# Kernel optimization log

Measured on AMD Instinct MI355X. Metric: run time of the kernel, lower is better.

## Reference

```python
import jax, jax.numpy as jnp
import numpy as np

N, D, H, E = 50000, 128, 64, 800000


def _linear_params(key, fan_in, fan_out):
    k1, k2 = jax.random.split(key)
    bound = 1.0 / np.sqrt(fan_in)
    w = jax.random.uniform(k1, (fan_in, fan_out), jnp.float32, -bound, bound)
    b = jax.random.uniform(k2, (fan_out,), jnp.float32, -bound, bound)
    return w, b


def setup_inputs() -> dict:
    key = jax.random.key(0)
    ks = jax.random.split(key, 10)
    node_states = jax.random.normal(ks[0], (N, D), jnp.float32)
    capacities = jax.random.uniform(ks[1], (N,), jnp.float32)
    edge_index = jax.random.randint(ks[2], (2, E), 0, N, jnp.int64)
    # redistribution_net: Linear(2D->H), SiLU, Linear(H->H), SiLU, Linear(H->1)
    rw1, rb1 = _linear_params(ks[3], 2 * D, H)
    rw2, rb2 = _linear_params(ks[4], H, H)
    rw3, rb3 = _linear_params(ks[5], H, 1)
    # protection_net: Linear(D+1->H), SiLU, Linear(H->1)
    pw1, pb1 = _linear_params(ks[6], D + 1, H)
    pw2, pb2 = _linear_params(ks[7], H, 1)
    # post_jump_transform: Linear(D->D), Tanh
    tw, tb = _linear_params(ks[8], D, D)
    return dict(node_states=node_states, capacities=capacities, edge_index=edge_index,
                rw1=rw1, rb1=rb1, rw2=rw2, rb2=rb2, rw3=rw3, rb3=rb3,
                pw1=pw1, pb1=pb1, pw2=pw2, pb2=pb2, tw=tw, tb=tb)


def reference(node_states, capacities, edge_index,
              rw1, rb1, rw2, rb2, rw3, rb3,
              pw1, pb1, pw2, pb2, tw, tb):
    n = node_states.shape[0]
    # --- detect_jumps: protection_net(cat(states, capacities)) > 0 ---
    x = jnp.concatenate([node_states, capacities[:, None]], axis=-1)  # (N, D+1)
    act = (jax.nn.silu(x @ pw1 + pb1) @ pw2 + pb2)[:, 0]              # (N,)
    jump_mask = act > 0.0

    # --- redistribute_load ---
    src, tgt = edge_index[0], edge_index[1]
    src_failed = jump_mask[src]
    tgt_alive = ~jump_mask[tgt]
    emask = src_failed & tgt_alive                                    # (E,)

    wi = jnp.concatenate([node_states[src], node_states[tgt]], axis=-1)  # (E, 2D)
    h = jax.nn.silu(wi @ rw1 + rb1)
    h = jax.nn.silu(h @ rw2 + rb2)
    raw = (h @ rw3 + rb3)[:, 0]                                       # (E,)

    # per-source segment softmax over edges with emask
    raw_m = jnp.where(emask, raw, -jnp.inf)
    seg_max = jax.ops.segment_max(raw_m, src, num_segments=n)
    seg_max = jnp.where(jnp.isfinite(seg_max), seg_max, 0.0)
    e = jnp.where(emask, jnp.exp(raw - seg_max[src]), 0.0)
    denom = jax.ops.segment_sum(e, src, num_segments=n)
    dsrc = denom[src]
    w = e / jnp.where(dsrc > 0, dsrc, 1.0)                            # (E,)

    failed_load = jnp.where(jump_mask[:, None], node_states, 0.0)     # (N, D)
    messages = w[:, None] * failed_load[src]                          # (E, D)
    added = jax.ops.segment_sum(messages, tgt, num_segments=n)        # (N, D)
    redistributed = node_states + added

    # --- apply_jumps: failed nodes -> tanh(Linear(x)) * 0.05 ---
    protected = jnp.tanh(redistributed @ tw + tb) * 0.05
    new_states = jnp.where(jump_mask[:, None], protected, redistributed)
    return new_states, jump_mask
```

## Files before the change

kernel.cpp:

```cpp
#include <hip/hip_runtime.h>
#include <cmath>

#define D 128
#define HID 64

__device__ __forceinline__ float silu_f(float x) { return x / (1.0f + expf(-x)); }

__device__ __forceinline__ float4 fma4(float a, float4 w, float4 c) {
    c.x = fmaf(a, w.x, c.x); c.y = fmaf(a, w.y, c.y);
    c.z = fmaf(a, w.z, c.z); c.w = fmaf(a, w.w, c.w);
    return c;
}
__device__ __forceinline__ float4 silu4(float4 v) {
    v.x = silu_f(v.x); v.y = silu_f(v.y); v.z = silu_f(v.z); v.w = silu_f(v.w);
    return v;
}

__device__ __forceinline__ unsigned fenc(float f) {
    unsigned u = __float_as_uint(f);
    return (u & 0x80000000u) ? ~u : (u | 0x80000000u);
}
__device__ __forceinline__ float fdec(unsigned e) {
    unsigned u = (e & 0x80000000u) ? (e & 0x7FFFFFFFu) : ~e;
    return __uint_as_float(u);
}

#define INIT16(bp) { const float4* _b4 = reinterpret_cast<const float4*>(bp); \
    h0 = _b4[0]; h1 = _b4[1]; h2 = _b4[2]; h3 = _b4[3]; \
    h4 = _b4[4]; h5 = _b4[5]; h6 = _b4[6]; h7 = _b4[7]; \
    h8 = _b4[8]; h9 = _b4[9]; h10 = _b4[10]; h11 = _b4[11]; \
    h12 = _b4[12]; h13 = _b4[13]; h14 = _b4[14]; h15 = _b4[15]; }

#define SILU16() { h0 = silu4(h0); h1 = silu4(h1); h2 = silu4(h2); h3 = silu4(h3); \
    h4 = silu4(h4); h5 = silu4(h5); h6 = silu4(h6); h7 = silu4(h7); \
    h8 = silu4(h8); h9 = silu4(h9); h10 = silu4(h10); h11 = silu4(h11); \
    h12 = silu4(h12); h13 = silu4(h13); h14 = silu4(h14); h15 = silu4(h15); }

__device__ __forceinline__ void fd4(float4 h, float4 w, float& s0, float& s1, float& s2, float& s3) {
    s0 = fmaf(h.x, w.x, s0); s1 = fmaf(h.y, w.y, s1);
    s2 = fmaf(h.z, w.z, s2); s3 = fmaf(h.w, w.w, s3);
}
#define FD16(w4) { fd4(h0, w4[0], s0, s1, s2, s3);  fd4(h1, w4[1], s0, s1, s2, s3);  \
    fd4(h2, w4[2], s0, s1, s2, s3);  fd4(h3, w4[3], s0, s1, s2, s3);  \
    fd4(h4, w4[4], s0, s1, s2, s3);  fd4(h5, w4[5], s0, s1, s2, s3);  \
    fd4(h6, w4[6], s0, s1, s2, s3);  fd4(h7, w4[7], s0, s1, s2, s3);  \
    fd4(h8, w4[8], s0, s1, s2, s3);  fd4(h9, w4[9], s0, s1, s2, s3);  \
    fd4(h10, w4[10], s0, s1, s2, s3); fd4(h11, w4[11], s0, s1, s2, s3); \
    fd4(h12, w4[12], s0, s1, s2, s3); fd4(h13, w4[13], s0, s1, s2, s3); \
    fd4(h14, w4[14], s0, s1, s2, s3); fd4(h15, w4[15], s0, s1, s2, s3); }

__device__ __forceinline__ float accdot(float4 h, float4 w, float act) {
    act = fmaf(silu_f(h.x), w.x, act);
    act = fmaf(silu_f(h.y), w.y, act);
    act = fmaf(silu_f(h.z), w.z, act);
    act = fmaf(silu_f(h.w), w.w, act);
    return act;
}

__global__ void k_prep(const float* __restrict__ rw2, float* __restrict__ rw2T) {
    int i = blockIdx.x * blockDim.x + threadIdx.x;
    if (i < HID * HID) rw2T[i] = rw2[(i & (HID - 1)) * HID + (i >> 6)];
}

__global__ __launch_bounds__(256) void k_protect(
    const float* __restrict__ states, const float* __restrict__ caps,
    const float* __restrict__ pw1, const float* __restrict__ pb1,
    const float* __restrict__ pw2, const float* __restrict__ pb2,
    unsigned* __restrict__ mask, unsigned* __restrict__ mlist,
    unsigned* __restrict__ counters, float* __restrict__ outmask, int N) {
    __shared__ float wl[129 * 64];
    unsigned tid = threadIdx.x;
    {
        const float4* s4 = reinterpret_cast<const float4*>(pw1);
        float4* d4 = reinterpret_cast<float4*>(wl);
#pragma unroll
        for (int q = 0; q < 9; ++q) {
            unsigned idx = tid + q * 256u;
            if (idx < 2064u) d4[idx] = s4[idx];
        }
    }
    __syncthreads();
    unsigned nl = tid >> 2, g = tid & 3u;
    unsigned n = blockIdx.x * 64u + nl;
    bool active = n < (unsigned)N;
    unsigned nq = active ? n : (unsigned)(N - 1);
    const float4* row = reinterpret_cast<const float4*>(states + (size_t)nq * D);
    float4 a0, a1, a2, a3;
    { const float4* b4 = reinterpret_cast<const float4*>(pb1 + g * 16);
      a0 = b4[0]; a1 = b4[1]; a2 = b4[2]; a3 = b4[3]; }
    const float* wg = wl + g * 16;
#pragma unroll 4
    for (int kb = 0; kb < 32; ++kb) {
        float4 x = row[kb];
        const float* w = wg + (size_t)kb * 4 * HID;
        const float4* w0 = reinterpret_cast<const float4*>(w);
        const float4* w1 = reinterpret_cast<const float4*>(w + HID);
        const float4* w2q = reinterpret_cast<const float4*>(w + 2 * HID);
        const float4* w3q = reinterpret_cast<const float4*>(w + 3 * HID);
        a0 = fma4(x.x, w0[0], a0); a1 = fma4(x.x, w0[1], a1); a2 = fma4(x.x, w0[2], a2); a3 = fma4(x.x, w0[3], a3);
        a0 = fma4(x.y, w1[0], a0); a1 = fma4(x.y, w1[1], a1); a2 = fma4(x.y, w1[2], a2); a3 = fma4(x.y, w1[3], a3);
        a0 = fma4(x.z, w2q[0], a0); a1 = fma4(x.z, w2q[1], a1); a2 = fma4(x.z, w2q[2], a2); a3 = fma4(x.z, w2q[3], a3);
        a0 = fma4(x.w, w3q[0], a0); a1 = fma4(x.w, w3q[1], a1); a2 = fma4(x.w, w3q[2], a2); a3 = fma4(x.w, w3q[3], a3);
    }
    {
        float xv = caps[nq];
        const float4* wc = reinterpret_cast<const float4*>(wg + (size_t)128 * HID);
        a0 = fma4(xv, wc[0], a0); a1 = fma4(xv, wc[1], a1);
        a2 = fma4(xv, wc[2], a2); a3 = fma4(xv, wc[3], a3);
    }
    const float4* w2 = reinterpret_cast<const float4*>(pw2 + g * 16);
    float p = 0.0f;
    p = accdot(a0, w2[0], p); p = accdot(a1, w2[1], p);
    p = accdot(a2, w2[2], p); p = accdot(a3, w2[3], p);
    p += __shfl_xor(p, 1);
    p += __shfl_xor(p, 2);
    bool pred = false;
    if (active && g == 0) {
        float act = p + pb2[0];
        unsigned m = (act > 0.0f) ? 1u : 0u;
        mask[n] = m;
        outmask[n] = m ? 1.0f : 0.0f;
        pred = (m != 0u);
    }
    unsigned lane = tid & 63u;
    unsigned long long bal = __ballot(pred);
    unsigned wcnt = (unsigned)__popcll(bal);
    unsigned pre  = (unsigned)__popcll(bal & ((1ull << lane) - 1ull));
    unsigned base = 0;
    if (lane == 0 && wcnt) base = atomicAdd(&counters[1], wcnt);
    base = __shfl(base, 0);
    if (pred) mlist[base + pre] = n;
}

__global__ __launch_bounds__(256) void k_nodemlp(
    const float* __restrict__ states, const unsigned* __restrict__ mask,
    const float* __restrict__ rw1, float* __restrict__ uv, int N) {
    __shared__ float wl[16384];
    unsigned tid = threadIdx.x;
    {
        const float4* s4 = reinterpret_cast<const float4*>(rw1);
        float4* d4 = reinterpret_cast<float4*>(wl);
#pragma unroll
        for (int q = 0; q < 16; ++q) d4[tid + q * 256u] = s4[tid + q * 256u];
    }
    __syncthreads();
    unsigned nl = tid >> 2, g = tid & 3u;
    unsigned n = blockIdx.x * 64u + nl;
    if (n >= (unsigned)N) return;
    const float4* row = reinterpret_cast<const float4*>(states + (size_t)n * D);
    unsigned m = mask[n];
    const float* wg = wl + (m ? 0u : 8192u) + g * 16;
    float4 a0, a1, a2, a3;
    a0.x=a0.y=a0.z=a0.w=0.f; a1=a0; a2=a0; a3=a0;
#pragma unroll 4
    for (int kb = 0; kb < 32; ++kb) {
        float4 x = row[kb];
        const float* w = wg + (size_t)kb * 4 * HID;
        const float4* w0 = reinterpret_cast<const float4*>(w);
        const float4* w1 = reinterpret_cast<const float4*>(w + HID);
        const float4* w2q = reinterpret_cast<const float4*>(w + 2 * HID);
        const float4* w3q = reinterpret_cast<const float4*>(w + 3 * HID);
        a0 = fma4(x.x, w0[0], a0); a1 = fma4(x.x, w0[1], a1); a2 = fma4(x.x, w0[2], a2); a3 = fma4(x.x, w0[3], a3);
        a0 = fma4(x.y, w1[0], a0); a1 = fma4(x.y, w1[1], a1); a2 = fma4(x.y, w1[2], a2); a3 = fma4(x.y, w1[3], a3);
        a0 = fma4(x.z, w2q[0], a0); a1 = fma4(x.z, w2q[1], a1); a2 = fma4(x.z, w2q[2], a2); a3 = fma4(x.z, w2q[3], a3);
        a0 = fma4(x.w, w3q[0], a0); a1 = fma4(x.w, w3q[1], a1); a2 = fma4(x.w, w3q[2], a2); a3 = fma4(x.w, w3q[3], a3);
    }
    float4* o = reinterpret_cast<float4*>(uv + (size_t)n * HID + g * 16);
    o[0] = a0; o[1] = a1; o[2] = a2; o[3] = a3;
}

__global__ __launch_bounds__(256) void k_compact(
    const int* __restrict__ ei, const unsigned* __restrict__ mask,
    unsigned* __restrict__ act_eid, unsigned* __restrict__ counters,
    unsigned* __restrict__ hist, int E) {
    __shared__ unsigned wbase[4];
    int e = blockIdx.x * 256 + threadIdx.x;
    unsigned wid = threadIdx.x >> 6, lane = threadIdx.x & 63u;
    bool pred = false; int t = 0;
    if (e < E) {
        int s = ei[e]; t = ei[E + e];
        pred = mask[s] && !mask[t];
    }
    unsigned long long bal = __ballot(pred);
    unsigned wcnt = (unsigned)__popcll(bal);
    unsigned pre  = (unsigned)__popcll(bal & ((1ull << lane) - 1ull));
    if (lane == 0) wbase[wid] = wcnt;
    __syncthreads();
    if (threadIdx.x == 0) {
        unsigned c0 = wbase[0], c1 = wbase[1], c2 = wbase[2], c3 = wbase[3];
        unsigned tot = c0 + c1 + c2 + c3;
        unsigned b = tot ? atomicAdd(&counters[0], tot) : 0u;
        wbase[0] = b; wbase[1] = b + c0; wbase[2] = b + c0 + c1; wbase[3] = b + c0 + c1 + c2;
    }
    __syncthreads();
    if (pred) {
        act_eid[wbase[wid] + pre] = (unsigned)e;
        atomicAdd(&hist[t], 1u);
    }
}

__global__ __launch_bounds__(256) void k_scanA(const unsigned* __restrict__ hist,
                                               unsigned* __restrict__ bsum, int N) {
    __shared__ unsigned sm[256];
    unsigned t = threadIdx.x;
    unsigned i = blockIdx.x * 256u + t;
    sm[t] = (i < (unsigned)N) ? hist[i] : 0u;
    __syncthreads();
#pragma unroll
    for (unsigned d = 128; d > 0; d >>= 1) {
        if (t < d) sm[t] += sm[t + d];
        __syncthreads();
    }
    if (t == 0) bsum[blockIdx.x] = sm[0];
}
__global__ __launch_bounds__(256) void k_scanB(const unsigned* __restrict__ bsum,
                                               unsigned* __restrict__ bpre, int nb) {
    __shared__ unsigned sm[256];
    unsigned t = threadIdx.x;
    unsigned v = (t < (unsigned)nb) ? bsum[t] : 0u;
    sm[t] = v;
    __syncthreads();
    for (unsigned d = 1; d < 256; d <<= 1) {
        unsigned x = (t >= d) ? sm[t - d] : 0u;
        __syncthreads();
        sm[t] += x;
        __syncthreads();
    }
    if (t < (unsigned)nb) bpre[t] = sm[t] - v;
}
__global__ __launch_bounds__(256) void k_scanC(const unsigned* __restrict__ hist,
                                               const unsigned* __restrict__ bpre,
                                               unsigned* __restrict__ offs,
                                               unsigned* __restrict__ cursor, int N) {
    __shared__ unsigned sm[256];
    unsigned t = threadIdx.x;
    unsigned i = blockIdx.x * 256u + t;
    unsigned v = (i < (unsigned)N) ? hist[i] : 0u;
    sm[t] = v;
    __syncthreads();
    for (unsigned d = 1; d < 256; d <<= 1) {
        unsigned x = (t >= d) ? sm[t - d] : 0u;
        __syncthreads();
        sm[t] += x;
        __syncthreads();
    }
    unsigned exc = sm[t] - v + bpre[blockIdx.x];
    if (i < (unsigned)N) { offs[i] = exc; cursor[i] = exc; }
    if (i == (unsigned)N - 1) offs[N] = exc + v;
}

__global__ __launch_bounds__(256) void k_edge_mlp(
    const float* __restrict__ uv, const int* __restrict__ ei,
    const float* __restrict__ rb1, const float* __restrict__ rw2T,
    const float* __restrict__ rb2, const float* __restrict__ rw3,
    const float* __restrict__ rb3,
    const unsigned* __restrict__ act_eid, const unsigned* __restrict__ counters,
    float* __restrict__ rawbuf, unsigned* __restrict__ segmax, int E) {
    unsigned cnt = counters[0];
    if (blockIdx.x * 256u >= cnt) return;
    unsigned tid = threadIdx.x;
    unsigned grp = blockIdx.x * 256u + tid;
    bool active = grp < cnt;
    unsigned gq = active ? grp : (cnt - 1);
    int e = (int)act_eid[gq];
    int s = ei[e], tg = ei[E + e];
    const float4* ur = reinterpret_cast<const float4*>(uv + (size_t)s * HID);
    const float4* vr = reinterpret_cast<const float4*>(uv + (size_t)tg * HID);
    float4 h0, h1, h2, h3, h4, h5, h6, h7, h8, h9, h10, h11, h12, h13, h14, h15;
    INIT16(rb1);
#define ADDUV(hh, i) { float4 _u = ur[i]; float4 _v = vr[i]; \
    hh.x = hh.x + _u.x + _v.x; hh.y = hh.y + _u.y + _v.y; \
    hh.z = hh.z + _u.z + _v.z; hh.w = hh.w + _u.w + _v.w; }
    ADDUV(h0, 0)  ADDUV(h1, 1)  ADDUV(h2, 2)  ADDUV(h3, 3)
    ADDUV(h4, 4)  ADDUV(h5, 5)  ADDUV(h6, 6)  ADDUV(h7, 7)
    ADDUV(h8, 8)  ADDUV(h9, 9)  ADDUV(h10, 10) ADDUV(h11, 11)
    ADDUV(h12, 12) ADDUV(h13, 13) ADDUV(h14, 14) ADDUV(h15, 15)
#undef ADDUV
    SILU16();
    float raw = rb3[0];
#pragma unroll 1
    for (int j = 0; j < HID; ++j) {
        const float4* w4 = reinterpret_cast<const float4*>(rw2T + (size_t)j * HID);
        float s0 = rb2[j], s1 = 0.f, s2 = 0.f, s3 = 0.f;
        FD16(w4);
        float h2v = silu_f((s0 + s1) + (s2 + s3));
        raw = fmaf(h2v, rw3[j], raw);
    }
    if (active) {
        rawbuf[grp] = raw;
        atomicMax(&segmax[s], fenc(raw));
    }
}

__global__ void k_expfill(const int* __restrict__ ei, const unsigned* __restrict__ act_eid,
                          const unsigned* __restrict__ counters, const unsigned* __restrict__ segmax,
                          const float* __restrict__ rawbuf, float* __restrict__ denom,
                          unsigned* __restrict__ cursor,
                          float* __restrict__ wbuf, unsigned* __restrict__ sbuf, int E) {
    unsigned t = blockIdx.x * blockDim.x + threadIdx.x;
    if (blockIdx.x * blockDim.x >= counters[0]) return;
    if (t >= counters[0]) return;
    int e = (int)act_eid[t];
    int s = ei[e], tg = ei[E + e];
    float ev = expf(rawbuf[t] - fdec(segmax[s]));
    atomicAdd(&denom[s], ev);
    unsigned pos = atomicAdd(&cursor[tg], 1u);
    wbuf[pos] = ev;
    sbuf[pos] = (unsigned)s;
}

__global__ __launch_bounds__(256) void k_gather(
    const float* __restrict__ states, const float* __restrict__ wbuf,
    const unsigned* __restrict__ sbuf, const unsigned* __restrict__ offs,
    const float* __restrict__ denom, const unsigned* __restrict__ mask,
    float* __restrict__ out, int N) {
    unsigned n = blockIdx.x * 4u + (threadIdx.x >> 6);
    unsigned lane = threadIdx.x & 63u;
    if (n >= (unsigned)N) return;
    if (mask[n]) return;
    unsigned start = offs[n], end = offs[n + 1];
    float2 acc = reinterpret_cast<const float2*>(states + (size_t)n * D)[lane];
    for (unsigned i = start; i < end; ++i) {
        unsigned s = sbuf[i];
        float w = wbuf[i] / denom[s];
        float2 sv = reinterpret_cast<const float2*>(states + (size_t)s * D)[lane];
        acc.x = fmaf(w, sv.x, acc.x);
        acc.y = fmaf(w, sv.y, acc.y);
    }
    reinterpret_cast<float2*>(out + (size_t)n * D)[lane] = acc;
}

__global__ __launch_bounds__(256) void k_jump(
    const float* __restrict__ states,
    const float* __restrict__ tw, const float* __restrict__ tb,
    const unsigned* __restrict__ mlist, const unsigned* __restrict__ counters,
    float* __restrict__ out) {
    __shared__ float xs[8][D];
    unsigned cnt = counters[1];
    unsigned base = blockIdx.x * 8u;
    if (base >= cnt || cnt == 0) return;
    unsigned tid = threadIdx.x;
    unsigned d = tid & 127u, r = tid >> 7;
    {
        unsigned j = tid >> 5;
        unsigned c = (tid & 31u) * 4u;
        unsigned slot = base + j; if (slot >= cnt) slot = cnt - 1;
        int nn = (int)mlist[slot];
        *reinterpret_cast<float4*>(&xs[j][c]) =
            *reinterpret_cast<const float4*>(&states[(size_t)nn * D + c]);
    }
    __syncthreads();
    float tbd = tb[d];
    float a0 = tbd, a1 = tbd, a2 = tbd, a3 = tbd;
    const float* x0 = &xs[r * 4 + 0][0];
    const float* x1 = &xs[r * 4 + 1][0];
    const float* x2 = &xs[r * 4 + 2][0];
    const float* x3 = &xs[r * 4 + 3][0];
#pragma unroll 1
    for (int k = 0; k < D; ++k) {
        float w = tw[(size_t)k * D + d];
        a0 = fmaf(x0[k], w, a0);
        a1 = fmaf(x1[k], w, a1);
        a2 = fmaf(x2[k], w, a2);
        a3 = fmaf(x3[k], w, a3);
    }
    float res[4] = {a0, a1, a2, a3};
#pragma unroll
    for (int j2 = 0; j2 < 4; ++j2) {
        unsigned slot = base + r * 4 + j2;
        if (slot < cnt) {
            int nn = (int)mlist[slot];
            out[(size_t)nn * D + d] = tanhf(res[j2]) * 0.05f;
        }
    }
}

extern "C" void kernel_launch(void* const* d_in, const int* in_sizes, int n_in,
                              void* d_out, int out_size, void* d_ws, size_t ws_size,
                              hipStream_t stream) {
    const float* states = (const float*)d_in[0];
    const float* caps   = (const float*)d_in[1];
    const int*   ei     = (const int*)d_in[2];
    const float* rw1 = (const float*)d_in[3];  const float* rb1 = (const float*)d_in[4];
    const float* rw2 = (const float*)d_in[5];  const float* rb2 = (const float*)d_in[6];
    const float* rw3 = (const float*)d_in[7];  const float* rb3 = (const float*)d_in[8];
    const float* pw1 = (const float*)d_in[9];  const float* pb1 = (const float*)d_in[10];
    const float* pw2 = (const float*)d_in[11]; const float* pb2 = (const float*)d_in[12];
    const float* tw  = (const float*)d_in[13]; const float* tb  = (const float*)d_in[14];
    const int N = in_sizes[1];
    const int E = in_sizes[2] / 2;
    float* out = (float*)d_out;
    const int nb = (N + 255) / 256;

    float* uv = out;

    unsigned* ws       = (unsigned*)d_ws;
    unsigned* counters = ws;
    unsigned* segmax   = ws + 4;
    float*    denom    = (float*)(ws + 4 + 1 * (size_t)N);
    unsigned* hist     = ws + 4 + 2 * (size_t)N;
    unsigned* mask     = ws + 4 + 3 * (size_t)N;
    unsigned* mlist    = ws + 4 + 4 * (size_t)N;
    unsigned* offs     = ws + 4 + 5 * (size_t)N;
    unsigned* cursor   = ws + 4 + 6 * (size_t)N + 1;
    unsigned* bsum     = ws + 4 + 7 * (size_t)N + 1;
    unsigned* bpre     = bsum + 256;
    unsigned* act_eid  = bpre + 256;
    float*    rawbuf   = (float*)(act_eid + (size_t)E);
    float*    wbuf     = (float*)(act_eid + 2 * (size_t)E);
    unsigned* sbuf     = act_eid + 3 * (size_t)E;
    float*    rw2T     = (float*)(act_eid + 4 * (size_t)E);

    (void)hipMemsetAsync(d_ws, 0, (size_t)(4 + 3 * (size_t)N) * 4, stream);

    k_prep<<<(HID * HID + 255) / 256, 256, 0, stream>>>(rw2, rw2T);
    k_protect<<<(N + 63) / 64, 256, 0, stream>>>(states, caps, pw1, pb1, pw2, pb2,
                                                 mask, mlist, counters, out + (size_t)N * D, N);
    k_nodemlp<<<(N + 63) / 64, 256, 0, stream>>>(states, mask, rw1, uv, N);
    k_compact<<<(E + 255) / 256, 256, 0, stream>>>(ei, mask, act_eid, counters, hist, E);
    k_scanA<<<nb, 256, 0, stream>>>(hist, bsum, N);
    k_scanB<<<1, 256, 0, stream>>>(bsum, bpre, nb);
    k_scanC<<<nb, 256, 0, stream>>>(hist, bpre, offs, cursor, N);
    k_edge_mlp<<<(E + 255) / 256, 256, 0, stream>>>(uv, ei, rb1, rw2T, rb2, rw3, rb3,
                                                    act_eid, counters, rawbuf, segmax, E);
    k_expfill<<<(E + 255) / 256, 256, 0, stream>>>(ei, act_eid, counters, segmax, rawbuf,
                                                   denom, cursor, wbuf, sbuf, E);
    k_gather<<<(N + 3) / 4, 256, 0, stream>>>(states, wbuf, sbuf, offs, denom, mask, out, N);
    k_jump<<<(N + 7) / 8, 256, 0, stream>>>(states, tw, tb, mlist, counters, out);
}
```

Before: 266.1 us.

## Fuse protect and node-MLP kernels; drop segment-max pass from softmax

Merges the protection-net kernel and the per-node first-layer projection into one kernel that reuses the shared-memory buffer, computing the mask in registers instead of rereading it. The edge MLP now computes exp(raw) directly and scatters weights and denominators, removing the segment-max atomic pass, the raw buffer and the separate expfill kernel. This saves two launches, a global round trip and a memset region. Without max subtraction, the softmax can overflow for large logits, so it relies on raw scores staying small.

Measured after the change: 256.3 us (median of 2 runs). -3.7%, faster.

```diff
diff --git a/kernel.cpp b/kernel.cpp
--- a/kernel.cpp
+++ b/kernel.cpp
@@ -14,15 +14,6 @@
 __device__ __forceinline__ float4 silu4(float4 v) {
     v.x = silu_f(v.x); v.y = silu_f(v.y); v.z = silu_f(v.z); v.w = silu_f(v.w);
     return v;
-}
-
-__device__ __forceinline__ unsigned fenc(float f) {
-    unsigned u = __float_as_uint(f);
-    return (u & 0x80000000u) ? ~u : (u | 0x80000000u);
-}
-__device__ __forceinline__ float fdec(unsigned e) {
-    unsigned u = (e & 0x80000000u) ? (e & 0x7FFFFFFFu) : ~e;
-    return __uint_as_float(u);
 }
 
 #define INIT16(bp) { const float4* _b4 = reinterpret_cast<const float4*>(bp); \
@@ -62,13 +53,15 @@
     if (i < HID * HID) rw2T[i] = rw2[(i & (HID - 1)) * HID + (i >> 6)];
 }
 
-__global__ __launch_bounds__(256) void k_protect(
+__global__ __launch_bounds__(256) void k_node(
     const float* __restrict__ states, const float* __restrict__ caps,
     const float* __restrict__ pw1, const float* __restrict__ pb1,
     const float* __restrict__ pw2, const float* __restrict__ pb2,
+    const float* __restrict__ rw1,
     unsigned* __restrict__ mask, unsigned* __restrict__ mlist,
-    unsigned* __restrict__ counters, float* __restrict__ outmask, int N) {
-    __shared__ float wl[129 * 64];
+    unsigned* __restrict__ counters, float* __restrict__ outmask,
+    float* __restrict__ uv, int N) {
+    __shared__ float wl[16384];
     unsigned tid = threadIdx.x;
     {
         const float4* s4 = reinterpret_cast<const float4*>(pw1);
@@ -85,58 +78,55 @@
     bool active = n < (unsigned)N;
     unsigned nq = active ? n : (unsigned)(N - 1);
     const float4* row = reinterpret_cast<const float4*>(states + (size_t)nq * D);
-    float4 a0, a1, a2, a3;
-    { const float4* b4 = reinterpret_cast<const float4*>(pb1 + g * 16);
-      a0 = b4[0]; a1 = b4[1]; a2 = b4[2]; a3 = b4[3]; }
-    const float* wg = wl + g * 16;
+    unsigned m;
+    {
+        float4 a0, a1, a2, a3;
+        { const float4* b4 = reinterpret_cast<const float4*>(pb1 + g * 16);
+          a0 = b4[0]; a1 = b4[1]; a2 = b4[2]; a3 = b4[3]; }
+        const float* wg = wl + g * 16;
 #pragma unroll 4
-    for (int kb = 0; kb < 32; ++kb) {
-        float4 x = row[kb];
-        const float* w = wg + (size_t)kb * 4 * HID;
-        const float4* w0 = reinterpret_cast<const float4*>(w);
-        const float4* w1 = reinterpret_cast<const float4*>(w + HID);
-        const float4* w2q = reinterpret_cast<const float4*>(w + 2 * HID);
-        const float4* w3q = reinterpret_cast<const float4*>(w + 3 * HID);
-        a0 = fma4(x.x, w0[0], a0); a1 = fma4(x.x, w0[1], a1); a2 = fma4(x.x, w0[2], a2); a3 = fma4(x.x, w0[3], a3);
-        a0 = fma4(x.y, w1[0], a0); a1 = fma4(x.y, w1[1], a1); a2 = fma4(x.y, w1[2], a2); a3 = fma4(x.y, w1[3], a3);
-        a0 = fma4(x.z, w2q[0], a0); a1 = fma4(x.z, w2q[1], a1); a2 = fma4(x.z, w2q[2], a2); a3 = fma4(x.z, w2q[3], a3);
-        a0 = fma4(x.w, w3q[0], a0); a1 = fma4(x.w, w3q[1], a1); a2 = fma4(x.w, w3q[2], a2); a3 = fma4(x.w, w3q[3], a3);
-    }
-    {
-        float xv = caps[nq];
-        const float4* wc = reinterpret_cast<const float4*>(wg + (size_t)128 * HID);
-        a0 = fma4(xv, wc[0], a0); a1 = fma4(xv, wc[1], a1);
-        a2 = fma4(xv, wc[2], a2); a3 = fma4(xv, wc[3], a3);
-    }
-    const float4* w2 = reinterpret_cast<const float4*>(pw2 + g * 16);
-    float p = 0.0f;
-    p = accdot(a0, w2[0], p); p = accdot(a1, w2[1], p);
-    p = accdot(a2, w2[2], p); p = accdot(a3, w2[3], p);
-    p += __shfl_xor(p, 1);
-    p += __shfl_xor(p, 2);
-    bool pred = false;
-    if (active && g == 0) {
+        for (int kb = 0; kb < 32; ++kb) {
+            float4 x = row[kb];
+            const float* w = wg + (size_t)kb * 4 * HID;
+            const float4* w0 = reinterpret_cast<const float4*>(w);
+            const float4* w1 = reinterpret_cast<const float4*>(w + HID);
+            const float4* w2q = reinterpret_cast<const float4*>(w + 2 * HID);
+            const float4* w3q = reinterpret_cast<const float4*>(w + 3 * HID);
+            a0 = fma4(x.x, w0[0], a0); a1 = fma4(x.x, w0[1], a1); a2 = fma4(x.x, w0[2], a2); a3 = fma4(x.x, w0[3], a3);
+            a0 = fma4(x.y, w1[0], a0); a1 = fma4(x.y, w1[1], a1); a2 = fma4(x.y, w1[2], a2); a3 = fma4(x.y, w1[3], a3);
+            a0 = fma4(x.z, w2q[0], a0); a1 = fma4(x.z, w2q[1], a1); a2 = fma4(x.z, w2q[2], a2); a3 = fma4(x.z, w2q[3], a3);
+            a0 = fma4(x.w, w3q[0], a0); a1 = fma4(x.w, w3q[1], a1); a2 = fma4(x.w, w3q[2], a2); a3 = fma4(x.w, w3q[3], a3);
+        }
+        {
+            float xv = caps[nq];
+            const float4* wc = reinterpret_cast<const float4*>(wg + (size_t)128 * HID);
+            a0 = fma4(xv, wc[0], a0); a1 = fma4(xv, wc[1], a1);
+            a2 = fma4(xv, wc[2], a2); a3 = fma4(xv, wc[3], a3);
+        }
+        const float4* w2 = reinterpret_cast<const float4*>(pw2 + g * 16);
+        float p = 0.0f;
+        p = accdot(a0, w2[0], p); p = accdot(a1, w2[1], p);
+        p = accdot(a2, w2[2], p); p = accdot(a3, w2[3], p);
+        p += __shfl_xor(p, 1);
+        p += __shfl_xor(p, 2);
         float act = p + pb2[0];
-        unsigned m = (act > 0.0f) ? 1u : 0u;
-        mask[n] = m;
-        outmask[n] = m ? 1.0f : 0.0f;
-        pred = (m != 0u);
-    }
-    unsigned lane = tid & 63u;
-    unsigned long long bal = __ballot(pred);
-    unsigned wcnt = (unsigned)__popcll(bal);
-    unsigned pre  = (unsigned)__popcll(bal & ((1ull << lane) - 1ull));
-    unsigned base = 0;
-    if (lane == 0 && wcnt) base = atomicAdd(&counters[1], wcnt);
-    base = __shfl(base, 0);
-    if (pred) mlist[base + pre] = n;
-}
-
-__global__ __launch_bounds__(256) void k_nodemlp(
-    const float* __restrict__ states, const unsigned* __restrict__ mask,
-    const float* __restrict__ rw1, float* __restrict__ uv, int N) {
-    __shared__ float wl[16384];
-    unsigned tid = threadIdx.x;
+        m = (act > 0.0f) ? 1u : 0u;
+        bool pred = false;
+        if (active && g == 0) {
+            mask[n] = m;
+            outmask[n] = m ? 1.0f : 0.0f;
+            pred = (m != 0u);
+        }
+        unsigned lane = tid & 63u;
+        unsigned long long bal = __ballot(pred);
+        unsigned wcnt = (unsigned)__popcll(bal);
+        unsigned pre  = (unsigned)__popcll(bal & ((1ull << lane) - 1ull));
+        unsigned base = 0;
+        if (lane == 0 && wcnt) base = atomicAdd(&counters[1], wcnt);
+        base = __shfl(base, 0);
+        if (pred) mlist[base + pre] = n;
+    }
+    __syncthreads();
     {
         const float4* s4 = reinterpret_cast<const float4*>(rw1);
         float4* d4 = reinterpret_cast<float4*>(wl);
@@ -144,11 +134,7 @@
         for (int q = 0; q < 16; ++q) d4[tid + q * 256u] = s4[tid + q * 256u];
     }
     __syncthreads();
-    unsigned nl = tid >> 2, g = tid & 3u;
-    unsigned n = blockIdx.x * 64u + nl;
-    if (n >= (unsigned)N) return;
-    const float4* row = reinterpret_cast<const float4*>(states + (size_t)n * D);
-    unsigned m = mask[n];
+    if (!active) return;
     const float* wg = wl + (m ? 0u : 8192u) + g * 16;
     float4 a0, a1, a2, a3;
     a0.x=a0.y=a0.z=a0.w=0.f; a1=a0; a2=a0; a3=a0;
@@ -255,7 +241,8 @@
     const float* __restrict__ rb2, const float* __restrict__ rw3,
     const float* __restrict__ rb3,
     const unsigned* __restrict__ act_eid, const unsigned* __restrict__ counters,
-    float* __restrict__ rawbuf, unsigned* __restrict__ segmax, int E) {
+    float* __restrict__ denom, unsigned* __restrict__ cursor,
+    float* __restrict__ wbuf, unsigned* __restrict__ sbuf, int E) {
     unsigned cnt = counters[0];
     if (blockIdx.x * 256u >= cnt) return;
     unsigned tid = threadIdx.x;
@@ -287,26 +274,12 @@
         raw = fmaf(h2v, rw3[j], raw);
     }
     if (active) {
-        rawbuf[grp] = raw;
-        atomicMax(&segmax[s], fenc(raw));
-    }
-}
-
-__global__ void k_expfill(const int* __restrict__ ei, const unsigned* __restrict__ act_eid,
-                          const unsigned* __restrict__ counters, const unsigned* __restrict__ segmax,
-                          const float* __restrict__ rawbuf, float* __restrict__ denom,
-                          unsigned* __restrict__ cursor,
-                          float* __restrict__ wbuf, unsigned* __restrict__ sbuf, int E) {
-    unsigned t = blockIdx.x * blockDim.x + threadIdx.x;
-    if (blockIdx.x * blockDim.x >= counters[0]) return;
-    if (t >= counters[0]) return;
-    int e = (int)act_eid[t];
-    int s = ei[e], tg = ei[E + e];
-    float ev = expf(rawbuf[t] - fdec(segmax[s]));
-    atomicAdd(&denom[s], ev);
-    unsigned pos = atomicAdd(&cursor[tg], 1u);
-    wbuf[pos] = ev;
-    sbuf[pos] = (unsigned)s;
+        float ev = expf(raw);
+        atomicAdd(&denom[s], ev);
+        unsigned pos = atomicAdd(&cursor[tg], 1u);
+        wbuf[pos] = ev;
+        sbuf[pos] = (unsigned)s;
+    }
 }
 
 __global__ __launch_bounds__(256) void k_gather(
@@ -396,35 +369,31 @@
 
     unsigned* ws       = (unsigned*)d_ws;
     unsigned* counters = ws;
-    unsigned* segmax   = ws + 4;
-    float*    denom    = (float*)(ws + 4 + 1 * (size_t)N);
-    unsigned* hist     = ws + 4 + 2 * (size_t)N;
-    unsigned* mask     = ws + 4 + 3 * (size_t)N;
-    unsigned* mlist    = ws + 4 + 4 * (size_t)N;
-    unsigned* offs     = ws + 4 + 5 * (size_t)N;
-    unsigned* cursor   = ws + 4 + 6 * (size_t)N + 1;
-    unsigned* bsum     = ws + 4 + 7 * (size_t)N + 1;
+    float*    denom    = (float*)(ws + 4);
+    unsigned* hist     = ws + 4 + 1 * (size_t)N;
+    unsigned* mask     = ws + 4 + 2 * (size_t)N;
+    unsigned* mlist    = ws + 4 + 3 * (size_t)N;
+    unsigned* offs     = ws + 4 + 4 * (size_t)N;
+    unsigned* cursor   = ws + 4 + 5 * (size_t)N + 1;
+    unsigned* bsum     = ws + 4 + 6 * (size_t)N + 1;
     unsigned* bpre     = bsum + 256;
     unsigned* act_eid  = bpre + 256;
-    float*    rawbuf   = (float*)(act_eid + (size_t)E);
-    float*    wbuf     = (float*)(act_eid + 2 * (size_t)E);
-    unsigned* sbuf     = act_eid + 3 * (size_t)E;
-    float*    rw2T     = (float*)(act_eid + 4 * (size_t)E);
-
-    (void)hipMemsetAsync(d_ws, 0, (size_t)(4 + 3 * (size_t)N) * 4, stream);
+    float*    wbuf     = (float*)(act_eid + (size_t)E);
+    unsigned* sbuf     = act_eid + 2 * (size_t)E;
+    float*    rw2T     = (float*)(act_eid + 3 * (size_t)E);
+
+    (void)hipMemsetAsync(d_ws, 0, (size_t)(4 + 2 * (size_t)N) * 4, stream);
 
     k_prep<<<(HID * HID + 255) / 256, 256, 0, stream>>>(rw2, rw2T);
-    k_protect<<<(N + 63) / 64, 256, 0, stream>>>(states, caps, pw1, pb1, pw2, pb2,
-                                                 mask, mlist, counters, out + (size_t)N * D, N);
-    k_nodemlp<<<(N + 63) / 64, 256, 0, stream>>>(states, mask, rw1, uv, N);
+    k_node<<<(N + 63) / 64, 256, 0, stream>>>(states, caps, pw1, pb1, pw2, pb2, rw1,
+                                              mask, mlist, counters, out + (size_t)N * D, uv, N);
     k_compact<<<(E + 255) / 256, 256, 0, stream>>>(ei, mask, act_eid, counters, hist, E);
     k_scanA<<<nb, 256, 0, stream>>>(hist, bsum, N);
     k_scanB<<<1, 256, 0, stream>>>(bsum, bpre, nb);
     k_scanC<<<nb, 256, 0, stream>>>(hist, bpre, offs, cursor, N);
     k_edge_mlp<<<(E + 255) / 256, 256, 0, stream>>>(uv, ei, rb1, rw2T, rb2, rw3, rb3,
-                                                    act_eid, counters, rawbuf, segmax, E);
-    k_expfill<<<(E + 255) / 256, 256, 0, stream>>>(ei, act_eid, counters, segmax, rawbuf,
-                                                   denom, cursor, wbuf, sbuf, E);
+                                                    act_eid, counters, denom, cursor,
+                                                    wbuf, sbuf, E);
     k_gather<<<(N + 3) / 4, 256, 0, stream>>>(states, wbuf, sbuf, offs, denom, mask, out, N);
     k_jump<<<(N + 7) / 8, 256, 0, stream>>>(states, tw, tb, mlist, counters, out);
 }
```
